# Optimization experiments

Measured on AMD Instinct MI355X. Metric: run time of the kernel, lower is better.

Reference implementation:

```python
import jax, jax.numpy as jnp
import numpy as np

LN_EPS = 1e-5
N_HEADS = 8

def _ln(x, g, b):
    mu = jnp.mean(x, axis=-1, keepdims=True)
    var = jnp.var(x, axis=-1, keepdims=True)
    return (x - mu) * jax.lax.rsqrt(var + LN_EPS) * g + b

def _glu(x):
    a, b = jnp.split(x, 2, axis=-1)
    return a * jax.nn.sigmoid(b)

def setup_inputs() -> dict:
    key = jax.random.key(0)
    ks = iter(jax.random.split(key, 48))
    B, C, HW, p = 16, 3, 224, 16
    d, N, M = 512, 2048, 25
    Sa, So, O, T = 512, 1024, 1000, 16
    P = (HW // p) ** 2
    rn = lambda shape, s=1.0: jax.random.normal(next(ks), shape, jnp.float32) * s
    inp = {
        'x': rn((B, C, HW, HW)),
        'conv_w': rn((d, C, p, p), 0.02), 'conv_b': jnp.zeros((d,)),
        'patch_ln_g': jnp.ones((d,)), 'patch_ln_b': jnp.zeros((d,)),
        'pos': rn((1, P, d), 0.02),
        'kv_w': rn((d, d), d ** -0.5), 'kv_b': jnp.zeros((d,)),
        'kv_ln_g': jnp.ones((d,)), 'kv_ln_b': jnp.zeros((d,)),
        'q_w': rn((d, Sa), Sa ** -0.5), 'q_b': jnp.zeros((d,)),
        'attn_in_w': rn((3 * d, d), d ** -0.5), 'attn_in_b': jnp.zeros((3 * d,)),
        'attn_out_w': rn((d, d), d ** -0.5), 'attn_out_b': jnp.zeros((d,)),
        'syn_w': rn((2 * N, d + N), (d + N) ** -0.5), 'syn_b': jnp.zeros((2 * N,)),
        'syn_ln_g': jnp.ones((N,)), 'syn_ln_b': jnp.zeros((N,)),
        'fc1_w': rn((N, M, 256), (2.0 / M) ** 0.5), 'fc1_b': jnp.zeros((N, 256)),
        'fc2_w': rn((N, 128, 2), (2.0 / 128) ** 0.5), 'fc2_b': jnp.zeros((N, 2)),
        'nlm_T': jnp.ones((1,)),
        'start_state': rn((N,), (1.0 / N) ** 0.5),
        'start_trace': rn((N, M), (1.0 / (N + M)) ** 0.5),
        'decay_action': jnp.zeros((Sa,)), 'decay_out': jnp.zeros((So,)),
        'out_w': rn((O, So), So ** -0.5), 'out_b': jnp.zeros((O,)),
        'act_left': jax.random.randint(next(ks), (Sa,), 0, N, jnp.int32),
        'act_right': jax.random.randint(next(ks), (Sa,), 0, N, jnp.int32),
        'out_left': jax.random.randint(next(ks), (So,), 0, N, jnp.int32),
        'out_right': jax.random.randint(next(ks), (So,), 0, N, jnp.int32),
        'ticks': T,
    }
    return inp

def _forward(x, conv_w, conv_b, patch_ln_g, patch_ln_b, pos, kv_w, kv_b, kv_ln_g, kv_ln_b,
             q_w, q_b, attn_in_w, attn_in_b, attn_out_w, attn_out_b,
             syn_w, syn_b, syn_ln_g, syn_ln_b, fc1_w, fc1_b, fc2_w, fc2_b, nlm_T,
             start_state, start_trace, decay_action, decay_out, out_w, out_b,
             act_left, act_right, out_left, out_right, ticks):
    B = x.shape[0]
    d = conv_w.shape[0]
    hd = d // N_HEADS
    scale = 1.0 / (hd ** 0.5)
    # --- patch embedding: Conv2d(stride=patch) -> flatten -> LN, then +pos ---
    pt = jax.lax.conv_general_dilated(
        x, conv_w, (conv_w.shape[2], conv_w.shape[3]), 'VALID',
        dimension_numbers=('NCHW', 'OIHW', 'NCHW')) + conv_b[None, :, None, None]
    pt = pt.reshape(B, d, -1).transpose(0, 2, 1)            # (B, P, d)
    pt = _ln(pt, patch_ln_g, patch_ln_b) + pos
    kv = _ln(pt @ kv_w.T + kv_b, kv_ln_g, kv_ln_b)          # (B, P, d)
    wq, wk, wv = jnp.split(attn_in_w, 3)
    bq, bk, bv = jnp.split(attn_in_b, 3)
    k = (kv @ wk.T + bk).reshape(B, -1, N_HEADS, hd)        # (B, P, H, hd)
    v = (kv @ wv.T + bv).reshape(B, -1, N_HEADS, hd)
    r_a = jnp.exp(-decay_action)
    r_o = jnp.exp(-decay_out)

    def sync(act, alpha, beta, r, left, right):
        pair = act[:, left] * act[:, right]                 # (B, S)
        alpha = r * alpha + pair
        beta = r * beta + 1.0
        return alpha * jax.lax.rsqrt(beta), alpha, beta

    def nlm(trace):
        h1 = _glu(jnp.einsum('bnm,nmh->bnh', trace, fc1_w) + fc1_b)  # (B, N, 128)
        h2 = _glu(jnp.einsum('bnh,nho->bno', h1, fc2_w) + fc2_b)     # (B, N, 1)
        return h2[..., 0] / nlm_T[0]

    act0 = jnp.broadcast_to(start_state, (B,) + start_state.shape)
    trace0 = jnp.broadcast_to(start_trace, (B,) + start_trace.shape)
    Sa = act_left.shape[0]
    So = out_left.shape[0]
    _, ao0, bo0 = sync(act0, jnp.zeros((B, So)), jnp.zeros((B, So)), r_o, out_left, out_right)
    carry0 = (trace0, act0, jnp.zeros((B, Sa)), jnp.zeros((B, Sa)), ao0, bo0)

    def step(carry, _):
        trace, act, aa, ba, ao, bo = carry
        s_act, aa, ba = sync(act, aa, ba, r_a, act_left, act_right)
        qv = s_act @ q_w.T + q_b                            # (B, d)
        qh = (qv @ wq.T + bq).reshape(B, N_HEADS, hd) * scale
        attn_w = jax.nn.softmax(jnp.einsum('bhd,bphd->bhp', qh, k), axis=-1)
        attn = jnp.einsum('bhp,bphd->bhd', attn_w, v).reshape(B, d) @ attn_out_w.T + attn_out_b
        pre = jnp.concatenate([attn, act], axis=-1)         # (B, d+N)
        state = _ln(_glu(pre @ syn_w.T + syn_b), syn_ln_g, syn_ln_b)  # (B, N)
        trace = jnp.concatenate([trace[:, :, 1:], state[:, :, None]], axis=-1)
        act = nlm(trace)
        s_out, ao, bo = sync(act, ao, bo, r_o, out_left, out_right)
        pred = s_out @ out_w.T + out_b                      # (B, out_dims)
        return (trace, act, aa, ba, ao, bo), pred

    _, preds = jax.lax.scan(step, carry0, None, length=ticks)
    preds = jnp.moveaxis(preds, 0, -1)                      # (B, out_dims, ticks)
    probs = jax.nn.softmax(preds, axis=1)
    ent = -jnp.sum(probs * jnp.log(probs + 1e-10), axis=1) / jnp.log(float(preds.shape[1]))
    return preds, ent

def reference(x, conv_w, conv_b, patch_ln_g, patch_ln_b, pos, kv_w, kv_b, kv_ln_g, kv_ln_b,
              q_w, q_b, attn_in_w, attn_in_b, attn_out_w, attn_out_b,
              syn_w, syn_b, syn_ln_g, syn_ln_b, fc1_w, fc1_b, fc2_w, fc2_b, nlm_T,
              start_state, start_trace, decay_action, decay_out, out_w, out_b,
              act_left, act_right, out_left, out_right, ticks):
    return _forward(x, conv_w, conv_b, patch_ln_g, patch_ln_b, pos, kv_w, kv_b, kv_ln_g, kv_ln_b,
                    q_w, q_b, attn_in_w, attn_in_b, attn_out_w, attn_out_b,
                    syn_w, syn_b, syn_ln_g, syn_ln_b, fc1_w, fc1_b, fc2_w, fc2_b, nlm_T,
                    start_state, start_trace, decay_action, decay_out, out_w, out_b,
                    act_left, act_right, out_left, out_right, ticks)
```

## Files before the change

### kernel.cpp

```cpp
#include <hip/hip_runtime.h>
#include <hip/hip_bf16.h>
#include <math.h>


#define DEV __device__ __forceinline__
typedef const float* fp;
typedef const float4* f4p;

#define B_   16
#define P_   196
#define D_   512
#define H_   8
#define HD_  64
#define N_   2048
#define M_   25
#define SA_  512
#define SO_  1024
#define O_   1000
#define T_   16

DEV float sigmf(float x){ return 1.0f / (1.0f + expf(-x)); }
DEV float wred(float v) { for (int m = 32; m; m >>= 1) v += __shfl_xor(v, m); return v; }
DEV float f4dot(float4 a, float4 b) { return a.x*b.x + a.y*b.y + a.z*b.z + a.w*b.w; }

DEV float breduce_sum(float v, float* red) {
  int t = threadIdx.x;
  red[t] = v; __syncthreads();
  for (int s = 128; s > 0; s >>= 1) {
    if (t < s) red[t] += red[t + s];
    __syncthreads();
  }
  float r = red[0]; __syncthreads();
  return r;
}
DEV float breduce_max(float v, float* red) {
  int t = threadIdx.x;
  red[t] = v; __syncthreads();
  for (int s = 128; s > 0; s >>= 1) {
    if (t < s) red[t] = fmaxf(red[t], red[t + s]);
    __syncthreads();
  }
  float r = red[0]; __syncthreads();
  return r;
}

__global__ __launch_bounds__(256) void k_patch_tile(fp x, fp conv_w, fp conv_b, float* pt) {
  int i0 = blockIdx.x * 64;
  int j0 = blockIdx.y * 64;
  int tid = threadIdx.x;
  int ti = tid >> 4, tj = tid & 15;
  __shared__ float As[64][17];
  __shared__ float Bs[64][17];
  float acc[4][4] = {{0,0,0,0},{0,0,0,0},{0,0,0,0},{0,0,0,0}};
  int p_loc = tid >> 2, k4 = (tid & 3) * 4;
  int bp = i0 + p_loc;
  int b = bp / P_, p = bp % P_;
  int ph = p / 14, pw = p % 14;
  const float* xbase = x + (size_t)b*3*224*224 + (size_t)(ph*16)*224 + pw*16;
  for (int kc = 0; kc < 48; kc++) {
    int ci = kc >> 4, qi = kc & 15;
    float4 av = *(f4p)(xbase + ((size_t)ci*224 + qi)*224 + k4);
    As[p_loc][k4+0] = av.x; As[p_loc][k4+1] = av.y;
    As[p_loc][k4+2] = av.z; As[p_loc][k4+3] = av.w;
    float4 bv = *(f4p)(conv_w + (size_t)(j0 + p_loc)*768 + kc*16 + k4);
    Bs[p_loc][k4+0] = bv.x; Bs[p_loc][k4+1] = bv.y;
    Bs[p_loc][k4+2] = bv.z; Bs[p_loc][k4+3] = bv.w;
    __syncthreads();
    for (int kk = 0; kk < 16; kk++) {
      float a0 = As[ti*4+0][kk], a1 = As[ti*4+1][kk];
      float a2 = As[ti*4+2][kk], a3 = As[ti*4+3][kk];
      float b0 = Bs[tj*4+0][kk], b1 = Bs[tj*4+1][kk];
      float b2 = Bs[tj*4+2][kk], b3 = Bs[tj*4+3][kk];
      acc[0][0] += a0*b0; acc[0][1] += a0*b1; acc[0][2] += a0*b2; acc[0][3] += a0*b3;
      acc[1][0] += a1*b0; acc[1][1] += a1*b1; acc[1][2] += a1*b2; acc[1][3] += a1*b3;
      acc[2][0] += a2*b0; acc[2][1] += a2*b1; acc[2][2] += a2*b2; acc[2][3] += a2*b3;
      acc[3][0] += a3*b0; acc[3][1] += a3*b1; acc[3][2] += a3*b2; acc[3][3] += a3*b3;
    }
    __syncthreads();
  }
  for (int ii = 0; ii < 4; ii++)
    for (int jj = 0; jj < 4; jj++)
      pt[(size_t)(i0 + ti*4 + ii)*D_ + j0 + tj*4 + jj] = acc[ii][jj] + conv_b[j0 + tj*4 + jj];
}

__global__ __launch_bounds__(256) void k_pln(float* pt, fp g, fp bb, fp pos) {
  int bp0 = blockIdx.x * 16;
  int tid = threadIdx.x, wave = tid >> 6, lane = tid & 63;
  for (int i = 0; i < 4; i++) {
    int bp = bp0 + wave*4 + i;
    int p = bp % P_;
    float* row = pt + (size_t)bp*D_;
    float4 v0 = *(f4p)(row + lane*8);
    float4 v1 = *(f4p)(row + lane*8 + 4);
    float s = v0.x+v0.y+v0.z+v0.w + v1.x+v1.y+v1.z+v1.w;
    float q = f4dot(v0,v0) + f4dot(v1,v1);
    s = wred(s); q = wred(q);
    float mu = s / (float)D_;
    float var = q / (float)D_ - mu*mu;
    float rstd = 1.f / sqrtf(var + 1e-5f);
    for (int j = 0; j < 8; j++) {
      int c = lane*8 + j;
      float v = (j < 4) ? ((const float*)&v0)[j] : ((const float*)&v1)[j-4];
      row[c] = (v - mu)*rstd*g[c] + bb[c] + pos[p*D_ + c];
    }
  }
}

__global__ __launch_bounds__(256) void k_kv_tile(const float* ptin, fp kv_w, fp kv_b, float* kvraw) {
  int i0 = blockIdx.x * 64;
  int j0 = blockIdx.y * 64;
  int tid = threadIdx.x;
  int ti = tid >> 4, tj = tid & 15;
  __shared__ float As[64][17];
  __shared__ float Bs[64][17];
  float acc[4][4] = {{0,0,0,0},{0,0,0,0},{0,0,0,0},{0,0,0,0}};
  int p_loc = tid >> 2, k4 = (tid & 3) * 4;
  for (int kc = 0; kc < 32; kc++) {
    float4 av = *(f4p)(ptin + (size_t)(i0 + p_loc)*D_ + kc*16 + k4);
    As[p_loc][k4+0] = av.x; As[p_loc][k4+1] = av.y;
    As[p_loc][k4+2] = av.z; As[p_loc][k4+3] = av.w;
    float4 bv = *(f4p)(kv_w + (size_t)(j0 + p_loc)*D_ + kc*16 + k4);
    Bs[p_loc][k4+0] = bv.x; Bs[p_loc][k4+1] = bv.y;
    Bs[p_loc][k4+2] = bv.z; Bs[p_loc][k4+3] = bv.w;
    __syncthreads();
    for (int kk = 0; kk < 16; kk++) {
      float a0 = As[ti*4+0][kk], a1 = As[ti*4+1][kk];
      float a2 = As[ti*4+2][kk], a3 = As[ti*4+3][kk];
      float b0 = Bs[tj*4+0][kk], b1 = Bs[tj*4+1][kk];
      float b2 = Bs[tj*4+2][kk], b3 = Bs[tj*4+3][kk];
      acc[0][0] += a0*b0; acc[0][1] += a0*b1; acc[0][2] += a0*b2; acc[0][3] += a0*b3;
      acc[1][0] += a1*b0; acc[1][1] += a1*b1; acc[1][2] += a1*b2; acc[1][3] += a1*b3;
      acc[2][0] += a2*b0; acc[2][1] += a2*b1; acc[2][2] += a2*b2; acc[2][3] += a2*b3;
      acc[3][0] += a3*b0; acc[3][1] += a3*b1; acc[3][2] += a3*b2; acc[3][3] += a3*b3;
    }
    __syncthreads();
  }
  for (int ii = 0; ii < 4; ii++)
    for (int jj = 0; jj < 4; jj++)
      kvraw[(size_t)(i0 + ti*4 + ii)*D_ + j0 + tj*4 + jj] = acc[ii][jj] + kv_b[j0 + tj*4 + jj];
}

__global__ __launch_bounds__(256) void k_kvln(float* kv, fp g, fp bb) {
  int bp0 = blockIdx.x * 16;
  int tid = threadIdx.x, wave = tid >> 6, lane = tid & 63;
  for (int i = 0; i < 4; i++) {
    int bp = bp0 + wave*4 + i;
    float* row = kv + (size_t)bp*D_;
    float4 v0 = *(f4p)(row + lane*8);
    float4 v1 = *(f4p)(row + lane*8 + 4);
    float s = v0.x+v0.y+v0.z+v0.w + v1.x+v1.y+v1.z+v1.w;
    float q = f4dot(v0,v0) + f4dot(v1,v1);
    s = wred(s); q = wred(q);
    float mu = s / (float)D_;
    float var = q / (float)D_ - mu*mu;
    float rstd = 1.f / sqrtf(var + 1e-5f);
    for (int j = 0; j < 8; j++) {
      int c = lane*8 + j;
      float v = (j < 4) ? ((const float*)&v0)[j] : ((const float*)&v1)[j-4];
      row[c] = (v - mu)*rstd*g[c] + bb[c];
    }
  }
}

__global__ __launch_bounds__(256) void k_wqc(fp aw, fp q_w, float* W_qc) {
  int i0 = blockIdx.x * 16, s0 = blockIdx.y * 16;
  int tid = threadIdx.x, il = tid >> 4, sl = tid & 15;
  __shared__ float s_wq[16][129];
  __shared__ float s_qw[128][17];
  float acc = 0.f;
  for (int kc = 0; kc < 4; kc++) {
    int k0 = kc * 128;
    for (int idx = tid; idx < 2048; idx += 256) {
      int r = idx >> 7, c = idx & 127;
      s_wq[r][c] = aw[(size_t)(i0 + r)*512 + k0 + c];
    }
    for (int idx = tid; idx < 2048; idx += 256) {
      int r = idx >> 4, c = idx & 15;
      s_qw[r][c] = q_w[(size_t)(k0 + r)*512 + s0 + c];
    }
    __syncthreads();
    for (int kk = 0; kk < 128; kk++)
      acc += s_wq[il][kk] * s_qw[kk][sl];
    __syncthreads();
  }
  W_qc[(size_t)(i0 + il)*512 + s0 + sl] = 0.125f * acc;
}

__global__ __launch_bounds__(256) void k_wqcb(fp aw, fp q_b, fp ab, float* bc) {
  int i = blockIdx.x * 256 + threadIdx.x;
  float acc = ab[i];
  for (int j = 0; j < 512; j++) acc += aw[(size_t)i*512 + j] * q_b[j];
  bc[i] = 0.125f * acc;
}

__global__ void k_init(fp start_state, fp start_trace, const int* oL, const int* oR,
                       fp decay_a, fp decay_o,
                       float* act, float* trace, float* aaA, float* baA,
                       float* aoA, float* boA, float* r_a, float* r_o) {
  int gid = blockIdx.x * 256 + threadIdx.x;
  if (gid < B_*N_*M_) {
    int bn = gid / M_, m = gid % M_;
    int n = bn % N_;
    trace[gid] = start_trace[n*M_ + m];
  }
  if (gid < B_*N_) act[gid] = start_state[gid & (N_-1)];
  if (gid < B_*SA_) { aaA[gid] = 0.f; baA[gid] = 0.f; }
  if (gid < B_*SO_) {
    int s = gid & (SO_-1);
    aoA[gid] = start_state[oL[s]] * start_state[oR[s]];
    boA[gid] = 1.0f;
  }
  if (gid < SA_) r_a[gid] = expf(-decay_a[gid]);
  if (gid < SO_) r_o[gid] = expf(-decay_o[gid]);
}

__global__ __launch_bounds__(256) void k_attout(
    const float* act,
    float* aaA, float* aaB, float* baA, float* baB,
    float* aoA, float* aoB, float* boA, float* boB,
    const float* r_a, const float* r_o,
    const float* W_qc, const float* bc, const float* kvb,
    fp aw, fp ab, fp out_w, fp out_b,
    const int* aL, const int* aR, const int* oL, const int* oR,
    float* av_ws, float* out, int t) {
  __shared__ float smem[8448];
  int bid = blockIdx.x;
  int tid = threadIdx.x, wave = tid >> 6, lane = tid & 63;

  if (bid < 128) {
    const float* aaR = (t & 1) ? aaB : aaA;  float* aaW = (t & 1) ? aaA : aaB;
    const float* baR = (t & 1) ? baB : baA;  float* baW = (t & 1) ? baA : baB;
    int b = bid >> 3, h = bid & 7;
    float* sact = smem;
    float* qhh  = smem + 512;
    float* qt   = smem + 576;
    float* mW   = smem + 1088;
    float* lW   = smem + 1092;
    float* zzL  = smem + 1600;
    float* zpart= smem + 2112;
    for (int cc = 0; cc < 2; cc++) {
      int s = tid + cc*256;
      float r = r_a[s];
      float pair = act[b*N_ + aL[s]] * act[b*N_ + aR[s]];
      float a  = r*aaR[b*SA_ + s] + pair;
      float bt = r*baR[b*SA_ + s] + 1.0f;
      if (h == 0) { aaW[b*SA_ + s] = a; baW[b*SA_ + s] = bt; }
      sact[s] = a / sqrtf(bt);
    }
    __syncthreads();
    for (int k = 0; k < 16; k++) {
      int r = h*HD_ + wave*16 + k;
      const float* wr = W_qc + (size_t)r*512 + lane*4;
      float s = f4dot(*(f4p)(wr),       *(f4p)(&sact[lane*4]))
              + f4dot(*(f4p)(wr + 256), *(f4p)(&sact[lane*4 + 256]));
      s = wred(s);
      if (lane == 0) qhh[wave*16 + k] = s + bc[r];
    }
    __syncthreads();
    float acc0 = 0.f, acc1 = 0.f;
    for (int e = 0; e < HD_; e++) {
      float q = qhh[e];
      const float* ar = aw + (size_t)(512 + h*HD_ + e)*D_;
      acc0 += q * ar[tid];
      acc1 += q * ar[tid + 256];
    }
    qt[tid] = acc0; qt[tid + 256] = acc1;
    float kb = 0.f;
    for (int e = 0; e < HD_; e++) kb += qhh[e] * ab[512 + h*HD_ + e];
    __syncthreads();
    float qreg[8];
    for (int j = 0; j < 8; j++) qreg[j] = qt[lane*8 + j];
    float m = -1e30f, l = 0.f;
    float zz8[8] = {0,0,0,0,0,0,0,0};
    for (int p = wave*49; p < wave*49 + 49; p++) {
      const float* kvp = kvb + ((size_t)(b*P_ + p))*D_ + lane*8;
      float4 v0 = *(f4p)(kvp), v1 = *(f4p)(kvp + 4);
      float d = v0.x*qreg[0] + v0.y*qreg[1] + v0.z*qreg[2] + v0.w*qreg[3]
              + v1.x*qreg[4] + v1.y*qreg[5] + v1.z*qreg[6] + v1.w*qreg[7];
      d = wred(d);
      float s_p = d + kb;
      float m_new = fmaxf(m, s_p);
      float scale = expf(m - m_new);
      float e = expf(s_p - m_new);
      l = l*scale + e;
      zz8[0] = zz8[0]*scale + e*v0.x; zz8[1] = zz8[1]*scale + e*v0.y;
      zz8[2] = zz8[2]*scale + e*v0.z; zz8[3] = zz8[3]*scale + e*v0.w;
      zz8[4] = zz8[4]*scale + e*v1.x; zz8[5] = zz8[5]*scale + e*v1.y;
      zz8[6] = zz8[6]*scale + e*v1.z; zz8[7] = zz8[7]*scale + e*v1.w;
      m = m_new;
    }
    if (lane == 0) { mW[wave] = m; lW[wave] = l; }
    for (int j = 0; j < 8; j++) zpart[wave*512 + lane*8 + j] = zz8[j];
    __syncthreads();
    {
      float M0 = fmaxf(fmaxf(mW[0], mW[1]), fmaxf(mW[2], mW[3]));
      float f0 = expf(mW[0]-M0), f1 = expf(mW[1]-M0), f2 = expf(mW[2]-M0), f3 = expf(mW[3]-M0);
      float L = lW[0]*f0 + lW[1]*f1 + lW[2]*f2 + lW[3]*f3;
      float invL = 1.f / L;
      for (int cc = 0; cc < 2; cc++) {
        int c = tid + cc*256;
        zzL[c] = (zpart[c]*f0 + zpart[512 + c]*f1 + zpart[1024 + c]*f2 + zpart[1536 + c]*f3) * invL;
      }
    }
    __syncthreads();
    for (int k = 0; k < 16; k++) {
      int e2 = wave*16 + k;
      int r = 1024 + h*HD_ + e2;
      const float* wr = aw + (size_t)r*512 + lane*4;
      float s = f4dot(*(f4p)(wr),       *(f4p)(&zzL[lane*4]))
              + f4dot(*(f4p)(wr + 256), *(f4p)(&zzL[lane*4 + 256]));
      s = wred(s);
      if (lane == 0) av_ws[b*D_ + h*HD_ + e2] = s + ab[r];
    }
  } else if (t > 0) {
    int s_ = t - 1;
    const float* aoR = (s_ & 1) ? aoB : aoA;  float* aoW = (s_ & 1) ? aoA : aoB;
    const float* boR = (s_ & 1) ? boB : boA;  float* boW = (s_ & 1) ? boA : boB;
    int obid = bid - 128;
    int rb = obid >> 1, bg = obid & 1;
    float* s_sout = smem;
    for (int i = 0; i < 32; i++) {
      int idx = tid + i*256;
      int bb = idx >> 10, s = idx & 1023;
      int b = bg*8 + bb;
      float r = r_o[s];
      float pair = act[b*N_ + oL[s]] * act[b*N_ + oR[s]];
      float a  = r*aoR[b*SO_ + s] + pair;
      float bt = r*boR[b*SO_ + s] + 1.f;
      if (rb == 0) { aoW[b*SO_ + s] = a; boW[b*SO_ + s] = bt; }
      s_sout[bb*1024 + s] = a / sqrtf(bt);
    }
    __syncthreads();
    for (int k = 0; k < 5; k++) {
      int r = rb*20 + wave*5 + k;
      const float* wr = out_w + (size_t)r*1024 + lane*4;
      float4 w0 = *(f4p)(wr),       w1 = *(f4p)(wr + 256),
             w2 = *(f4p)(wr + 512), w3 = *(f4p)(wr + 768);
      float pp[8];
      for (int bb = 0; bb < 8; bb++) {
        const float* pb = &s_sout[bb*1024 + lane*4];
        pp[bb] = f4dot(w0, *(f4p)(pb))       + f4dot(w1, *(f4p)(pb + 256))
               + f4dot(w2, *(f4p)(pb + 512)) + f4dot(w3, *(f4p)(pb + 768));
      }
      float obr = out_b[r];
      for (int bb = 0; bb < 8; bb++) {
        float s = wred(pp[bb]);
        if (lane == 0) out[((size_t)((bg*8 + bb)*O_ + r))*T_ + s_] = s + obr;
      }
    }
  }
}

__global__ __launch_bounds__(256) void k_ao2(const float* av_ws, fp ow, fp ob, float* attn_o) {
  int rb = blockIdx.x, bg = blockIdx.y;
  int tid = threadIdx.x, wave = tid >> 6, lane = tid & 63;
  __shared__ float s_a[8][516];
  for (int idx = tid; idx < 8*512; idx += 256) {
    int bb = idx >> 9, c = idx & 511;
    s_a[bb][c] = av_ws[(bg*8 + bb)*D_ + c];
  }
  __syncthreads();
  for (int k = 0; k < 8; k++) {
    int r = rb*32 + wave*8 + k;
    const float* wr = ow + (size_t)r*512 + lane*4;
    float4 w0 = *(f4p)(wr), w1 = *(f4p)(wr + 256);
    float pp[8];
    for (int bb = 0; bb < 8; bb++) {
      const float* pb = &s_a[bb][lane*4];
      pp[bb] = f4dot(w0, *(f4p)(pb)) + f4dot(w1, *(f4p)(pb + 256));
    }
    float obr = ob[r];
    for (int bb = 0; bb < 8; bb++) {
      float s = wred(pp[bb]);
      if (lane == 0) attn_o[(bg*8 + bb)*D_ + r] = s + obr;
    }
  }
}

__global__ __launch_bounds__(256) void k_syn(const float* attn_o, const float* act,
                                             fp syn_w, fp syn_b, float* ysyn,
                                             float* psum, float* psq) {
  int rb = blockIdx.x, bg = blockIdx.y;
  int tid = threadIdx.x, wave = tid >> 6, lane = tid & 63;
  __shared__ float pre8[8*2560];
  __shared__ float wsum[4][8], wsq[4][8];
  for (int bb = 0; bb < 8; bb++) {
    int b = bg*8 + bb;
    for (int i = tid; i < 2560; i += 256)
      pre8[bb*2560 + i] = (i < 512) ? attn_o[b*D_ + i] : act[b*N_ + (i - 512)];
  }
  __syncthreads();
  float lsum[8] = {0,0,0,0,0,0,0,0}, lsq[8] = {0,0,0,0,0,0,0,0};
  for (int k = 0; k < 4; k++) {
    int pr = rb*16 + wave*4 + k;
    float sA[8];
    {
      const float* wr = syn_w + (size_t)pr*2560 + lane*4;
      float4 wreg[10];
      for (int j = 0; j < 10; j++) wreg[j] = *(f4p)(wr + j*256);
      float pp[8] = {0,0,0,0,0,0,0,0};
      for (int j = 0; j < 10; j++) {
        int idx = lane*4 + j*256;
        for (int bb = 0; bb < 8; bb++)
          pp[bb] += f4dot(wreg[j], *(f4p)(&pre8[bb*2560 + idx]));
      }
      float sb = syn_b[pr];
      for (int bb = 0; bb < 8; bb++) sA[bb] = wred(pp[bb]) + sb;
    }
    {
      int r2 = pr + 2048;
      const float* wr = syn_w + (size_t)r2*2560 + lane*4;
      float4 wreg[10];
      for (int j = 0; j < 10; j++) wreg[j] = *(f4p)(wr + j*256);
      float pp[8] = {0,0,0,0,0,0,0,0};
      for (int j = 0; j < 10; j++) {
        int idx = lane*4 + j*256;
        for (int bb = 0; bb < 8; bb++)
          pp[bb] += f4dot(wreg[j], *(f4p)(&pre8[bb*2560 + idx]));
      }
      float sb = syn_b[r2];
      for (int bb = 0; bb < 8; bb++) {
        float sG = wred(pp[bb]) + sb;
        float v = sA[bb] * sigmf(sG);
        lsum[bb] += v; lsq[bb] += v*v;
        if (lane == 0) ysyn[(size_t)(bg*8 + bb)*N_ + pr] = v;
      }
    }
  }
  if (lane == 0)
    for (int bb = 0; bb < 8; bb++) { wsum[wave][bb] = lsum[bb]; wsq[wave][bb] = lsq[bb]; }
  __syncthreads();
  if (tid < 8) {
    float s1 = wsum[0][tid] + wsum[1][tid] + wsum[2][tid] + wsum[3][tid];
    float s2 = wsq[0][tid]  + wsq[1][tid]  + wsq[2][tid]  + wsq[3][tid];
    psum[rb*16 + bg*8 + tid] = s1;
    psq [rb*16 + bg*8 + tid] = s2;
  }
}

__global__ __launch_bounds__(256) void k_nlm(float* trace, const float* ysyn,
                                             const float* psum, const float* psq,
                                             fp sg, fp sb2,
                                             fp fc1_w, fp fc1_b, fp fc2_w, fp fc2_b,
                                             fp nlmT, float* act) {
  int n = blockIdx.x, tid = threadIdx.x;
  __shared__ float tr[B_][M_];
  __shared__ float uu[256][17];
  __shared__ float h1[128][17];
  __shared__ float vout[B_][2];
  __shared__ float s_mu[16], s_rstd[16];
  {
    int b = tid >> 4, j = tid & 15;
    if (tid < 256) {
      float s1 = 0.f, s2 = 0.f;
      for (int rb = j; rb < 128; rb += 16) { s1 += psum[rb*16 + b]; s2 += psq[rb*16 + b]; }
      for (int m = 8; m; m >>= 1) { s1 += __shfl_xor(s1, m); s2 += __shfl_xor(s2, m); }
      if (j == 0) {
        float mu = s1 / (float)N_;
        s_mu[b] = mu;
        s_rstd[b] = 1.f / sqrtf(s2 / (float)N_ - mu*mu + 1e-5f);
      }
    }
  }
  __syncthreads();
  for (int i = tid; i < B_*M_; i += 256) {
    int b = i / M_, m = i % M_;
    float v;
    if (m < M_-1) v = trace[((size_t)(b*N_ + n))*M_ + m + 1];
    else          v = (ysyn[(size_t)b*N_ + n] - s_mu[b]) * s_rstd[b] * sg[n] + sb2[n];
    tr[b][m] = v;
  }
  __syncthreads();
  for (int i = tid; i < B_*M_; i += 256) {
    int b = i / M_, m = i % M_;
    trace[((size_t)(b*N_ + n))*M_ + m] = tr[b][m];
  }
  float w25[M_];
  for (int m = 0; m < M_; m++) w25[m] = fc1_w[((size_t)n*M_ + m)*256 + tid];
  float bias = fc1_b[n*256 + tid];
  for (int b = 0; b < B_; b++) {
    float u = bias;
    for (int m = 0; m < M_; m++) u += tr[b][m]*w25[m];
    uu[tid][b] = u;
  }
  __syncthreads();
  if (tid < 128) {
    for (int b = 0; b < B_; b++)
      h1[tid][b] = uu[tid][b] * sigmf(uu[tid + 128][b]);
  }
  __syncthreads();
  if (tid < 32) {
    int b = tid >> 1, o = tid & 1;
    float acc = fc2_b[n*2 + o];
    for (int hh = 0; hh < 128; hh++) acc += h1[hh][b] * fc2_w[((size_t)n*128 + hh)*2 + o];
    vout[b][o] = acc;
  }
  __syncthreads();
  if (tid < B_) {
    act[tid*N_ + n] = vout[tid][0] * sigmf(vout[tid][1]) / nlmT[0];
  }
}

__global__ __launch_bounds__(256) void k_out(const float* act, const float* aoR, const float* boR,
                                             float* aoW, float* boW, const float* r_o,
                                             const int* L, const int* R,
                                             fp out_w, fp out_b, float* out, int t) {
  int rb = blockIdx.x, bg = blockIdx.y;
  int tid = threadIdx.x, wave = tid >> 6, lane = tid & 63;
  __shared__ float s_sout[8][1024];
  for (int i = 0; i < 32; i++) {
    int idx = tid + i*256;
    int bb = idx >> 10, s = idx & 1023;
    int b = bg*8 + bb;
    float r = r_o[s];
    float pair = act[b*N_ + L[s]] * act[b*N_ + R[s]];
    float a  = r*aoR[b*SO_ + s] + pair;
    float bt = r*boR[b*SO_ + s] + 1.f;
    if (rb == 0) { aoW[b*SO_ + s] = a; boW[b*SO_ + s] = bt; }
    s_sout[bb][s] = a / sqrtf(bt);
  }
  __syncthreads();
  for (int k = 0; k < 5; k++) {
    int r = rb*20 + wave*5 + k;
    const float* wr = out_w + (size_t)r*1024 + lane*4;
    float4 w0 = *(f4p)(wr),       w1 = *(f4p)(wr + 256),
           w2 = *(f4p)(wr + 512), w3 = *(f4p)(wr + 768);
    float pp[8];
    for (int bb = 0; bb < 8; bb++) {
      const float* pb = &s_sout[bb][lane*4];
      pp[bb] = f4dot(w0, *(f4p)(pb))       + f4dot(w1, *(f4p)(pb + 256))
             + f4dot(w2, *(f4p)(pb + 512)) + f4dot(w3, *(f4p)(pb + 768));
    }
    float obr = out_b[r];
    for (int bb = 0; bb < 8; bb++) {
      float s = wred(pp[bb]);
      if (lane == 0) out[((size_t)((bg*8 + bb)*O_ + r))*T_ + t] = s + obr;
    }
  }
}

__global__ __launch_bounds__(256) void k_final(float* out) {
  int b = blockIdx.x, t = blockIdx.y, tid = threadIdx.x;
  __shared__ float red[256];
  float lm = -1e30f;
  for (int o = tid; o < O_; o += 256) lm = fmaxf(lm, out[((size_t)(b*O_ + o))*T_ + t]);
  float Mx = breduce_max(lm, red);
  float le = 0.f;
  for (int o = tid; o < O_; o += 256) le += expf(out[((size_t)(b*O_ + o))*T_ + t] - Mx);
  float S = breduce_sum(le, red);
  float lt = 0.f;
  for (int o = tid; o < O_; o += 256) {
    float pr = expf(out[((size_t)(b*O_ + o))*T_ + t] - Mx) / S;
    lt += pr * logf(pr + 1e-10f);
  }
  float E = breduce_sum(lt, red);
  if (tid == 0)
    out[(size_t)B_*O_*T_ + b*T_ + t] = -E / logf((float)O_);
}

extern "C" void kernel_launch(void* const* d_in, const int* in_sizes, int n_in,
                              void* d_out, int out_size, void* d_ws, size_t ws_size,
                              hipStream_t stream) {
  (void)in_sizes; (void)n_in; (void)out_size; (void)ws_size;
  fp x          = (fp)d_in[0];
  fp conv_w     = (fp)d_in[1];
  fp conv_b     = (fp)d_in[2];
  fp patch_ln_g = (fp)d_in[3];
  fp patch_ln_b = (fp)d_in[4];
  fp pos        = (fp)d_in[5];
  fp kv_w       = (fp)d_in[6];
  fp kv_b       = (fp)d_in[7];
  fp kv_ln_g    = (fp)d_in[8];
  fp kv_ln_b    = (fp)d_in[9];
  fp q_w        = (fp)d_in[10];
  fp q_b        = (fp)d_in[11];
  fp attn_in_w  = (fp)d_in[12];
  fp attn_in_b  = (fp)d_in[13];
  fp attn_out_w = (fp)d_in[14];
  fp attn_out_b = (fp)d_in[15];
  fp syn_w      = (fp)d_in[16];
  fp syn_b      = (fp)d_in[17];
  fp syn_ln_g   = (fp)d_in[18];
  fp syn_ln_b   = (fp)d_in[19];
  fp fc1_w      = (fp)d_in[20];
  fp fc1_b      = (fp)d_in[21];
  fp fc2_w      = (fp)d_in[22];
  fp fc2_b      = (fp)d_in[23];
  fp nlm_T      = (fp)d_in[24];
  fp start_state= (fp)d_in[25];
  fp start_trace= (fp)d_in[26];
  fp decay_a    = (fp)d_in[27];
  fp decay_o    = (fp)d_in[28];
  fp out_w      = (fp)d_in[29];
  fp out_b      = (fp)d_in[30];
  const int* act_left  = (const int*)d_in[31];
  const int* act_right = (const int*)d_in[32];
  const int* out_left  = (const int*)d_in[33];
  const int* out_right = (const int*)d_in[34];

  float* ws = (float*)d_ws;
  float* pt     = ws;
  float* act    = ws + 0;
  float* trace  = ws + 32768;
  float* aaA    = ws + 851968;
  float* aaB    = ws + 860160;
  float* baA    = ws + 868352;
  float* baB    = ws + 876544;
  float* aoA    = ws + 884736;
  float* aoB    = ws + 901120;
  float* boA    = ws + 917504;
  float* boB    = ws + 933888;
  float* attn_o = ws + 958464;
  float* ysyn   = ws + 966656;
  float* psum   = ws + 999424;
  float* psq    = ws + 1001472;
  float* av_ws  = ws + 1064960;
  float* r_a    = ws + 1073152;
  float* r_o    = ws + 1073664;
  float* W_qc   = ws + 1074688;
  float* bc     = ws + 1336832;
  float* kvb    = ws + 1605632;

  k_patch_tile<<<dim3(49, 8), dim3(256), 0, stream>>>(x, conv_w, conv_b, pt);
  k_pln<<<dim3(196), dim3(256), 0, stream>>>(pt, patch_ln_g, patch_ln_b, pos);
  k_kv_tile<<<dim3(49, 8), dim3(256), 0, stream>>>(pt, kv_w, kv_b, kvb);
  k_kvln<<<dim3(196), dim3(256), 0, stream>>>(kvb, kv_ln_g, kv_ln_b);
  k_wqc<<<dim3(32, 32), dim3(256), 0, stream>>>(attn_in_w, q_w, W_qc);
  k_wqcb<<<dim3(2), dim3(256), 0, stream>>>(attn_in_w, q_b, attn_in_b, bc);
  k_init<<<dim3((B_*N_*M_ + 255)/256), dim3(256), 0, stream>>>(start_state, start_trace,
        out_left, out_right, decay_a, decay_o, act, trace, aaA, baA, aoA, boA, r_a, r_o);

  for (int t = 0; t < T_; t++) {
    k_attout<<<dim3(228), dim3(256), 0, stream>>>(
        act, aaA, aaB, baA, baB, aoA, aoB, boA, boB, r_a, r_o,
        W_qc, bc, kvb, attn_in_w, attn_in_b, out_w, out_b,
        act_left, act_right, out_left, out_right, av_ws, (float*)d_out, t);
    k_ao2<<<dim3(16, 2), dim3(256), 0, stream>>>(av_ws, attn_out_w, attn_out_b, attn_o);
    k_syn<<<dim3(128, 2), dim3(256), 0, stream>>>(attn_o, act, syn_w, syn_b, ysyn, psum, psq);
    k_nlm<<<dim3(N_), dim3(256), 0, stream>>>(trace, ysyn, psum, psq, syn_ln_g, syn_ln_b,
                                              fc1_w, fc1_b, fc2_w, fc2_b, nlm_T, act);
  }
  {
    int t = T_ - 1;
    const float* aoR = (t & 1) ? aoB : aoA;  float* aoW = (t & 1) ? aoA : aoB;
    const float* boR = (t & 1) ? boB : boA;  float* boW = (t & 1) ? boA : boB;
    k_out<<<dim3(50, 2), dim3(256), 0, stream>>>(act, aoR, boR, aoW, boW, r_o,
                                                 out_left, out_right, out_w, out_b,
                                                 (float*)d_out, t);
  }
  k_final<<<dim3(16, 16), dim3(256), 0, stream>>>((float*)d_out);
}
```

Before: 2.976 ms.

## Fuse attention output projection into attout kernel via grid barrier, tidy tiles

```diff
diff --git a/kernel.cpp b/kernel.cpp
--- a/kernel.cpp
+++ b/kernel.cpp
@@ -18,6 +18,7 @@
 #define SO_  1024
 #define O_   1000
 #define T_   16
+#define AGRID_ 228
 
 DEV float sigmf(float x){ return 1.0f / (1.0f + expf(-x)); }
 DEV float wred(float v) { for (int m = 32; m; m >>= 1) v += __shfl_xor(v, m); return v; }
@@ -44,13 +45,23 @@
   return r;
 }
 
+DEV void gbar(unsigned int* bar, unsigned int target) {
+  __syncthreads();
+  if (threadIdx.x == 0) {
+    __hip_atomic_fetch_add(bar, 1u, __ATOMIC_ACQ_REL, __HIP_MEMORY_SCOPE_AGENT);
+    while (__hip_atomic_load(bar, __ATOMIC_ACQUIRE, __HIP_MEMORY_SCOPE_AGENT) < target)
+      __builtin_amdgcn_s_sleep(1);
+  }
+  __syncthreads();
+}
+
 __global__ __launch_bounds__(256) void k_patch_tile(fp x, fp conv_w, fp conv_b, float* pt) {
   int i0 = blockIdx.x * 64;
   int j0 = blockIdx.y * 64;
   int tid = threadIdx.x;
   int ti = tid >> 4, tj = tid & 15;
-  __shared__ float As[64][17];
-  __shared__ float Bs[64][17];
+  __shared__ float As[64][20];
+  __shared__ float Bs[64][20];
   float acc[4][4] = {{0,0,0,0},{0,0,0,0},{0,0,0,0},{0,0,0,0}};
   int p_loc = tid >> 2, k4 = (tid & 3) * 4;
   int bp = i0 + p_loc;
@@ -59,12 +70,8 @@
   const float* xbase = x + (size_t)b*3*224*224 + (size_t)(ph*16)*224 + pw*16;
   for (int kc = 0; kc < 48; kc++) {
     int ci = kc >> 4, qi = kc & 15;
-    float4 av = *(f4p)(xbase + ((size_t)ci*224 + qi)*224 + k4);
-    As[p_loc][k4+0] = av.x; As[p_loc][k4+1] = av.y;
-    As[p_loc][k4+2] = av.z; As[p_loc][k4+3] = av.w;
-    float4 bv = *(f4p)(conv_w + (size_t)(j0 + p_loc)*768 + kc*16 + k4);
-    Bs[p_loc][k4+0] = bv.x; Bs[p_loc][k4+1] = bv.y;
-    Bs[p_loc][k4+2] = bv.z; Bs[p_loc][k4+3] = bv.w;
+    *(float4*)&As[p_loc][k4] = *(f4p)(xbase + ((size_t)ci*224 + qi)*224 + k4);
+    *(float4*)&Bs[p_loc][k4] = *(f4p)(conv_w + (size_t)(j0 + p_loc)*768 + kc*16 + k4);
     __syncthreads();
     for (int kk = 0; kk < 16; kk++) {
       float a0 = As[ti*4+0][kk], a1 = As[ti*4+1][kk];
@@ -111,17 +118,13 @@
   int j0 = blockIdx.y * 64;
   int tid = threadIdx.x;
   int ti = tid >> 4, tj = tid & 15;
-  __shared__ float As[64][17];
-  __shared__ float Bs[64][17];
+  __shared__ float As[64][20];
+  __shared__ float Bs[64][20];
   float acc[4][4] = {{0,0,0,0},{0,0,0,0},{0,0,0,0},{0,0,0,0}};
   int p_loc = tid >> 2, k4 = (tid & 3) * 4;
   for (int kc = 0; kc < 32; kc++) {
-    float4 av = *(f4p)(ptin + (size_t)(i0 + p_loc)*D_ + kc*16 + k4);
-    As[p_loc][k4+0] = av.x; As[p_loc][k4+1] = av.y;
-    As[p_loc][k4+2] = av.z; As[p_loc][k4+3] = av.w;
-    float4 bv = *(f4p)(kv_w + (size_t)(j0 + p_loc)*D_ + kc*16 + k4);
-    Bs[p_loc][k4+0] = bv.x; Bs[p_loc][k4+1] = bv.y;
-    Bs[p_loc][k4+2] = bv.z; Bs[p_loc][k4+3] = bv.w;
+    *(float4*)&As[p_loc][k4] = *(f4p)(ptin + (size_t)(i0 + p_loc)*D_ + kc*16 + k4);
+    *(float4*)&Bs[p_loc][k4] = *(f4p)(kv_w + (size_t)(j0 + p_loc)*D_ + kc*16 + k4);
     __syncthreads();
     for (int kk = 0; kk < 16; kk++) {
       float a0 = As[ti*4+0][kk], a1 = As[ti*4+1][kk];
@@ -196,8 +199,9 @@
 __global__ void k_init(fp start_state, fp start_trace, const int* oL, const int* oR,
                        fp decay_a, fp decay_o,
                        float* act, float* trace, float* aaA, float* baA,
-                       float* aoA, float* boA, float* r_a, float* r_o) {
+                       float* aoA, float* boA, float* r_a, float* r_o, unsigned int* bar) {
   int gid = blockIdx.x * 256 + threadIdx.x;
+  if (gid == 0) *bar = 0u;
   if (gid < B_*N_*M_) {
     int bn = gid / M_, m = gid % M_;
     int n = bn % N_;
@@ -220,9 +224,9 @@
     float* aoA, float* aoB, float* boA, float* boB,
     const float* r_a, const float* r_o,
     const float* W_qc, const float* bc, const float* kvb,
-    fp aw, fp ab, fp out_w, fp out_b,
+    fp aw, fp ab, fp ow, fp ob, fp out_w, fp out_b,
     const int* aL, const int* aR, const int* oL, const int* oR,
-    float* av_ws, float* out, int t) {
+    float* av_ws, float* attn_o, float* out, unsigned int* bar, int t) {
   __shared__ float smem[8448];
   int bid = blockIdx.x;
   int tid = threadIdx.x, wave = tid >> 6, lane = tid & 63;
@@ -349,30 +353,32 @@
       }
     }
   }
-}
-
-__global__ __launch_bounds__(256) void k_ao2(const float* av_ws, fp ow, fp ob, float* attn_o) {
-  int rb = blockIdx.x, bg = blockIdx.y;
-  int tid = threadIdx.x, wave = tid >> 6, lane = tid & 63;
-  __shared__ float s_a[8][516];
-  for (int idx = tid; idx < 8*512; idx += 256) {
-    int bb = idx >> 9, c = idx & 511;
-    s_a[bb][c] = av_ws[(bg*8 + bb)*D_ + c];
-  }
-  __syncthreads();
-  for (int k = 0; k < 8; k++) {
-    int r = rb*32 + wave*8 + k;
-    const float* wr = ow + (size_t)r*512 + lane*4;
-    float4 w0 = *(f4p)(wr), w1 = *(f4p)(wr + 256);
-    float pp[8];
-    for (int bb = 0; bb < 8; bb++) {
-      const float* pb = &s_a[bb][lane*4];
-      pp[bb] = f4dot(w0, *(f4p)(pb)) + f4dot(w1, *(f4p)(pb + 256));
-    }
-    float obr = ob[r];
-    for (int bb = 0; bb < 8; bb++) {
-      float s = wred(pp[bb]);
-      if (lane == 0) attn_o[(bg*8 + bb)*D_ + r] = s + obr;
+
+  gbar(bar, (unsigned)AGRID_ * (unsigned)(t + 1));
+
+  if (bid < 32) {
+    int rb = bid >> 1, bg = bid & 1;
+    float* s_a = smem;
+    __syncthreads();
+    for (int idx = tid; idx < 8*512; idx += 256) {
+      int bb = idx >> 9, c = idx & 511;
+      s_a[bb*516 + c] = av_ws[(bg*8 + bb)*D_ + c];
+    }
+    __syncthreads();
+    for (int k = 0; k < 8; k++) {
+      int r = rb*32 + wave*8 + k;
+      const float* wr = ow + (size_t)r*512 + lane*4;
+      float4 w0 = *(f4p)(wr), w1 = *(f4p)(wr + 256);
+      float pp[8];
+      for (int bb = 0; bb < 8; bb++) {
+        const float* pb = &s_a[bb*516 + lane*4];
+        pp[bb] = f4dot(w0, *(f4p)(pb)) + f4dot(w1, *(f4p)(pb + 256));
+      }
+      float obr = ob[r];
+      for (int bb = 0; bb < 8; bb++) {
+        float s = wred(pp[bb]);
+        if (lane == 0) attn_o[(bg*8 + bb)*D_ + r] = s + obr;
+      }
     }
   }
 }
@@ -451,15 +457,13 @@
   __shared__ float s_mu[16], s_rstd[16];
   {
     int b = tid >> 4, j = tid & 15;
-    if (tid < 256) {
-      float s1 = 0.f, s2 = 0.f;
-      for (int rb = j; rb < 128; rb += 16) { s1 += psum[rb*16 + b]; s2 += psq[rb*16 + b]; }
-      for (int m = 8; m; m >>= 1) { s1 += __shfl_xor(s1, m); s2 += __shfl_xor(s2, m); }
-      if (j == 0) {
-        float mu = s1 / (float)N_;
-        s_mu[b] = mu;
-        s_rstd[b] = 1.f / sqrtf(s2 / (float)N_ - mu*mu + 1e-5f);
-      }
+    float s1 = 0.f, s2 = 0.f;
+    for (int rb = j; rb < 128; rb += 16) { s1 += psum[rb*16 + b]; s2 += psq[rb*16 + b]; }
+    for (int m = 8; m; m >>= 1) { s1 += __shfl_xor(s1, m); s2 += __shfl_xor(s2, m); }
+    if (j == 0) {
+      float mu = s1 / (float)N_;
+      s_mu[b] = mu;
+      s_rstd[b] = 1.f / sqrtf(s2 / (float)N_ - mu*mu + 1e-5f);
     }
   }
   __syncthreads();
@@ -505,19 +509,18 @@
                                              float* aoW, float* boW, const float* r_o,
                                              const int* L, const int* R,
                                              fp out_w, fp out_b, float* out, int t) {
-  int rb = blockIdx.x, bg = blockIdx.y;
+  int rb = blockIdx.x;
   int tid = threadIdx.x, wave = tid >> 6, lane = tid & 63;
-  __shared__ float s_sout[8][1024];
-  for (int i = 0; i < 32; i++) {
-    int idx = tid + i*256;
-    int bb = idx >> 10, s = idx & 1023;
-    int b = bg*8 + bb;
+  __shared__ float s_sout[16*1024];
+  for (int i = 0; i < 64; i++) {
+    int e = i*256 + tid;
+    int bb = e >> 10, s = e & 1023;
     float r = r_o[s];
-    float pair = act[b*N_ + L[s]] * act[b*N_ + R[s]];
-    float a  = r*aoR[b*SO_ + s] + pair;
-    float bt = r*boR[b*SO_ + s] + 1.f;
-    if (rb == 0) { aoW[b*SO_ + s] = a; boW[b*SO_ + s] = bt; }
-    s_sout[bb][s] = a / sqrtf(bt);
+    float pair = act[bb*N_ + L[s]] * act[bb*N_ + R[s]];
+    float a  = r*aoR[bb*SO_ + s] + pair;
+    float bt = r*boR[bb*SO_ + s] + 1.f;
+    if (rb == 0) { aoW[bb*SO_ + s] = a; boW[bb*SO_ + s] = bt; }
+    s_sout[bb*1024 + s] = a / sqrtf(bt);
   }
   __syncthreads();
   for (int k = 0; k < 5; k++) {
@@ -525,16 +528,16 @@
     const float* wr = out_w + (size_t)r*1024 + lane*4;
     float4 w0 = *(f4p)(wr),       w1 = *(f4p)(wr + 256),
            w2 = *(f4p)(wr + 512), w3 = *(f4p)(wr + 768);
-    float pp[8];
-    for (int bb = 0; bb < 8; bb++) {
-      const float* pb = &s_sout[bb][lane*4];
+    float pp[16];
+    for (int bb = 0; bb < 16; bb++) {
+      const float* pb = &s_sout[bb*1024 + lane*4];
       pp[bb] = f4dot(w0, *(f4p)(pb))       + f4dot(w1, *(f4p)(pb + 256))
              + f4dot(w2, *(f4p)(pb + 512)) + f4dot(w3, *(f4p)(pb + 768));
     }
     float obr = out_b[r];
-    for (int bb = 0; bb < 8; bb++) {
+    for (int bb = 0; bb < 16; bb++) {
       float s = wred(pp[bb]);
-      if (lane == 0) out[((size_t)((bg*8 + bb)*O_ + r))*T_ + t] = s + obr;
+      if (lane == 0) out[((size_t)(bb*O_ + r))*T_ + t] = s + obr;
     }
   }
 }
@@ -619,6 +622,7 @@
   float* r_o    = ws + 1073664;
   float* W_qc   = ws + 1074688;
   float* bc     = ws + 1336832;
+  unsigned int* bar = (unsigned int*)(ws + 1337344);
   float* kvb    = ws + 1605632;
 
   k_patch_tile<<<dim3(49, 8), dim3(256), 0, stream>>>(x, conv_w, conv_b, pt);
@@ -628,14 +632,13 @@
   k_wqc<<<dim3(32, 32), dim3(256), 0, stream>>>(attn_in_w, q_w, W_qc);
   k_wqcb<<<dim3(2), dim3(256), 0, stream>>>(attn_in_w, q_b, attn_in_b, bc);
   k_init<<<dim3((B_*N_*M_ + 255)/256), dim3(256), 0, stream>>>(start_state, start_trace,
-        out_left, out_right, decay_a, decay_o, act, trace, aaA, baA, aoA, boA, r_a, r_o);
+        out_left, out_right, decay_a, decay_o, act, trace, aaA, baA, aoA, boA, r_a, r_o, bar);
 
   for (int t = 0; t < T_; t++) {
-    k_attout<<<dim3(228), dim3(256), 0, stream>>>(
+    k_attout<<<dim3(AGRID_), dim3(256), 0, stream>>>(
         act, aaA, aaB, baA, baB, aoA, aoB, boA, boB, r_a, r_o,
-        W_qc, bc, kvb, attn_in_w, attn_in_b, out_w, out_b,
-        act_left, act_right, out_left, out_right, av_ws, (float*)d_out, t);
-    k_ao2<<<dim3(16, 2), dim3(256), 0, stream>>>(av_ws, attn_out_w, attn_out_b, attn_o);
+        W_qc, bc, kvb, attn_in_w, attn_in_b, attn_out_w, attn_out_b, out_w, out_b,
+        act_left, act_right, out_left, out_right, av_ws, attn_o, (float*)d_out, bar, t);
     k_syn<<<dim3(128, 2), dim3(256), 0, stream>>>(attn_o, act, syn_w, syn_b, ysyn, psum, psq);
     k_nlm<<<dim3(N_), dim3(256), 0, stream>>>(trace, ysyn, psum, psq, syn_ln_g, syn_ln_b,
                                               fc1_w, fc1_b, fc2_w, fc2_b, nlm_T, act);
@@ -644,9 +647,9 @@
     int t = T_ - 1;
     const float* aoR = (t & 1) ? aoB : aoA;  float* aoW = (t & 1) ? aoA : aoB;
     const float* boR = (t & 1) ? boB : boA;  float* boW = (t & 1) ? boA : boB;
-    k_out<<<dim3(50, 2), dim3(256), 0, stream>>>(act, aoR, boR, aoW, boW, r_o,
-                                                 out_left, out_right, out_w, out_b,
-                                                 (float*)d_out, t);
+    k_out<<<dim3(50), dim3(256), 0, stream>>>(act, aoR, boR, aoW, boW, r_o,
+                                              out_left, out_right, out_w, out_b,
+                                              (float*)d_out, t);
   }
   k_final<<<dim3(16, 16), dim3(256), 0, stream>>>((float*)d_out);
 }
```

Measured after the change: 3.638 ms. +22.3%, slower.
